# Optimization experiments

Hardware: AMD Instinct MI355X
Metric: run time of the kernel (lower is better)

The kernel has to match this reference:

```python
import jax, jax.numpy as jnp
import numpy as np

DIM = 768
HEADS = 12


def setup_inputs() -> dict:
    key = jax.random.key(0)
    ks = jax.random.split(key, 8)
    B, N, M, C, H = 8, 1024, 1024, DIM, HEADS
    x = jax.random.normal(ks[0], (B, N, C), dtype=jnp.float32)
    context = jax.random.normal(ks[1], (B, M, C), dtype=jnp.float32)
    s = 1.0 / np.sqrt(C)
    Wq = jax.random.normal(ks[2], (C, C), dtype=jnp.float32) * s
    Wkv = jax.random.normal(ks[3], (C, 2 * C), dtype=jnp.float32) * s
    # depthwise 3x3 conv over attention map: OIHW with I=1 (groups=H)
    conv_w = jax.random.normal(ks[4], (H, 1, 3, 3), dtype=jnp.float32) * (1.0 / 3.0)
    conv_b = jax.random.normal(ks[5], (H,), dtype=jnp.float32) * 0.02
    Wp = jax.random.normal(ks[6], (C, C), dtype=jnp.float32) * s
    bp = jax.random.normal(ks[7], (C,), dtype=jnp.float32) * 0.02
    return {"x": x, "context": context, "Wq": Wq, "Wkv": Wkv,
            "conv_w": conv_w, "conv_b": conv_b, "Wp": Wp, "bp": bp}


def reference(x, context, Wq, Wkv, conv_w, conv_b, Wp, bp):
    B, N, C = x.shape
    H = conv_w.shape[0]
    d = C // H
    scale = d ** (-0.5)
    # projections
    q = (x @ Wq).reshape(B, N, H, d).transpose(0, 2, 1, 3)          # [B,H,N,d]
    kv = (context @ Wkv).reshape(B, -1, 2, H, d)
    k = kv[:, :, 0].transpose(0, 2, 1, 3)                            # [B,H,M,d]
    v = kv[:, :, 1].transpose(0, 2, 1, 3)                            # [B,H,M,d]
    # attention scores + softmax over keys
    attn = jnp.einsum('bhnd,bhmd->bhnm', q, k) * scale               # [B,H,N,M]
    attn = jax.nn.softmax(attn, axis=-1)
    # depthwise 3x3 conv on the attention map (heads = channels)
    attn = jax.lax.conv_general_dilated(
        attn, conv_w, window_strides=(1, 1), padding='SAME',
        feature_group_count=H,
        dimension_numbers=('NCHW', 'OIHW', 'NCHW'))
    attn = attn + conv_b[None, :, None, None]
    # attend values, merge heads, output projection
    out = jnp.einsum('bhnm,bhmd->bhnd', attn, v)                     # [B,H,N,d]
    out = out.transpose(0, 2, 1, 3).reshape(B, N, C)
    return out @ Wp + bp
```

## Files before the change

### kernel.cpp

```cpp
#include <hip/hip_runtime.h>
#include <hip/hip_bf16.h>

typedef __hip_bfloat16 bf16;
typedef __hip_bfloat162 bf162;

#define B_ 8
#define N_ 1024
#define M_ 1024
#define C_ 768
#define H_ 12
#define D_ 64

typedef __attribute__((ext_vector_type(8))) short short8v;
typedef __attribute__((ext_vector_type(4))) float f32x4;

__device__ __forceinline__ float bf2f(bf16 v){ return __bfloat162float(v); }
__device__ __forceinline__ bf16 f2bf(float v){ return __float2bfloat16(v); }

__device__ __forceinline__ void gl_lds16(const bf16* g, bf16* l){
  __builtin_amdgcn_global_load_lds((const __attribute__((address_space(1))) unsigned*)g,
                                   (__attribute__((address_space(3))) unsigned*)l, 16, 0, 0);
}

__global__ __launch_bounds__(256)
void cvt_both(const float* __restrict__ x, const float* __restrict__ ctx,
              bf16* __restrict__ xb, bf16* __restrict__ ctxb){
  int i = blockIdx.x*256 + threadIdx.x;
  const float* src; bf16* dst; int j;
  if (i < 786432){ src = x;   dst = xb;   j = i; }
  else           { src = ctx; dst = ctxb; j = i - 786432; }
  const float4* ip = reinterpret_cast<const float4*>(src) + 2*(size_t)j;
  float4 a = ip[0], b = ip[1];
  union { uint4 u; bf16 h[8]; } pk;
  pk.h[0]=f2bf(a.x); pk.h[1]=f2bf(a.y); pk.h[2]=f2bf(a.z); pk.h[3]=f2bf(a.w);
  pk.h[4]=f2bf(b.x); pk.h[5]=f2bf(b.y); pk.h[6]=f2bf(b.z); pk.h[7]=f2bf(b.w);
  reinterpret_cast<uint4*>(dst)[j] = pk.u;
}

__global__ __launch_bounds__(256)
void transpose_all(const float* __restrict__ Wq, const float* __restrict__ Wkv,
                   const float* __restrict__ Wp,
                   bf16* __restrict__ Wqt, bf16* __restrict__ Wkvt, bf16* __restrict__ Wpt)
{
  __shared__ float tile[32][33];
  int bid = blockIdx.x;
  const float* W; bf16* Wt; int N, bx, by;
  if (bid < 576)       { W = Wq;  Wt = Wqt;  N = 768;  bx = bid % 24;  by = bid / 24; }
  else if (bid < 1728) { int r = bid - 576;  W = Wkv; Wt = Wkvt; N = 1536; bx = r % 48; by = r / 48; }
  else                 { int r = bid - 1728; W = Wp;  Wt = Wpt;  N = 768;  bx = r % 24; by = r / 24; }
  const int K = 768;
  const int n0 = bx*32, k0 = by*32;
  const int tx = threadIdx.x & 31, ty = threadIdx.x >> 5;
#pragma unroll
  for (int i=0;i<32;i+=8) tile[ty+i][tx] = W[(size_t)(k0+ty+i)*N + n0+tx];
  __syncthreads();
#pragma unroll
  for (int i=0;i<32;i+=8) Wt[(size_t)(n0+ty+i)*K + k0+tx] = f2bf(tile[tx][ty+i]);
}

__global__ __launch_bounds__(1024)
void yprep(bf16* __restrict__ Vt, bf16* __restrict__ Y0, bf16* __restrict__ Y1,
           float* __restrict__ SV, const float* __restrict__ conv_w)
{
  __shared__ bf16 sm[65536];
  const int t = threadIdx.x;
  const int bh = blockIdx.x;
  const int h = bh % H_;
  const size_t pbase = (size_t)bh * 65536;

  float w[9];
#pragma unroll
  for (int q=0;q<9;q++) w[q] = conv_w[h*9+q];

#pragma unroll
  for (int k=0;k<8;k++){
    int idx = k*8192 + t*8;
    *reinterpret_cast<uint4*>(&sm[idx]) = *reinterpret_cast<const uint4*>(Vt + pbase + idx);
  }
  __syncthreads();

  const int d = t >> 4;
  const int j = t & 15;
  const int xb = (d >> 1) & 3;
  float ssum = 0.f;
#pragma unroll
  for (int k=0;k<8;k++){
    const int moff = j*64 + k*8;
    const int base = d*1024 + moff;
    union { uint4 u; bf16 hh[8]; } mv;
    mv.u = *reinterpret_cast<const uint4*>(&sm[base]);
    float v[8];
#pragma unroll
    for (int e=0;e<8;e++) v[e] = bf2f(mv.hh[e]);
    float vl = (moff == 0)    ? 0.f : bf2f(sm[base-1]);
    float vr = (moff == 1016) ? 0.f : bf2f(sm[base+8]);

    union { uint4 u; bf16 hh[8]; } o0, o1, o2;
#pragma unroll
    for (int m=0;m<8;m++){
      float vm1 = (m==0) ? vl : v[m-1];
      float vp1 = (m==7) ? vr : v[m+1];
      o0.hh[m] = f2bf(w[0]*vp1 + w[1]*v[m] + w[2]*vm1);
      o1.hh[m] = f2bf(w[3]*vp1 + w[4]*v[m] + w[5]*vm1);
      o2.hh[m] = f2bf(w[6]*vp1 + w[7]*v[m] + w[8]*vm1);
      ssum += v[m];
    }
    const int blk = (moff >> 3) & 3;
    size_t go = pbase + ((size_t)(moff>>5)<<11) + d*32 + ((blk ^ xb)<<3);
    *reinterpret_cast<uint4*>(Y0 + go) = o0.u;
    *reinterpret_cast<uint4*>(Y1 + go) = o1.u;
    *reinterpret_cast<uint4*>(Vt + go) = o2.u;
  }

  ssum += __shfl_xor(ssum, 1);
  ssum += __shfl_xor(ssum, 2);
  ssum += __shfl_xor(ssum, 4);
  ssum += __shfl_xor(ssum, 8);
  if (j == 0) SV[bh*64 + d] = ssum;
}

__global__ __launch_bounds__(256)
void gemm_qkv(const bf16* __restrict__ A0, const bf16* __restrict__ A1,
              const bf16* __restrict__ Bt0, const bf16* __restrict__ Bt1,
              bf16* __restrict__ outQ, bf16* __restrict__ outK, bf16* __restrict__ outV)
{
  __shared__ bf16 As[128*32];
  __shared__ bf16 Bs[128*32];
  const int K = 768;

  const int nwg = 1152, cpx = nwg >> 3;
  int bid = blockIdx.x;
  bid = (bid & 7)*cpx + (bid >> 3);
  const int rowb = bid / 18, colb = bid - rowb*18;
  const int row0 = rowb*128;
  const bool isQ = (colb < 6);
  const int c0 = isQ ? colb*128 : (colb-6)*128;

  const int t = threadIdx.x;
  const int w = t>>6, l = t&63, lr = l&15, g = l>>4;
  const int wr = w>>1, wc = w&1;

  const bf16* Ap = (isQ ? A0 : A1) + (size_t)row0*K;
  const bf16* Bp = (isQ ? Bt0 : Bt1) + (size_t)c0*K;
  const int srow = t>>2;
  const int schunk = (t&3)*8;

  f32x4 acc[4][4];
#pragma unroll
  for (int mi=0;mi<4;mi++)
#pragma unroll
    for (int ni=0;ni<4;ni++) acc[mi][ni] = (f32x4){0.f,0.f,0.f,0.f};

  for (int k0 = 0; k0 < K; k0 += 32){
    gl_lds16(Ap + (size_t)srow*K      + k0 + schunk, As + t*8);
    gl_lds16(Ap + (size_t)(srow+64)*K + k0 + schunk, As + 2048 + t*8);
    gl_lds16(Bp + (size_t)srow*K      + k0 + schunk, Bs + t*8);
    gl_lds16(Bp + (size_t)(srow+64)*K + k0 + schunk, Bs + 2048 + t*8);
    __syncthreads();

    short8v a[4], b[4];
#pragma unroll
    for (int mi=0;mi<4;mi++)
      a[mi] = *reinterpret_cast<const short8v*>(&As[(wr*64+mi*16+lr)*32 + g*8]);
#pragma unroll
    for (int ni=0;ni<4;ni++)
      b[ni] = *reinterpret_cast<const short8v*>(&Bs[(wc*64+ni*16+lr)*32 + g*8]);
#pragma unroll
    for (int mi=0;mi<4;mi++)
#pragma unroll
      for (int ni=0;ni<4;ni++)
        acc[mi][ni] = __builtin_amdgcn_mfma_f32_16x16x32_bf16(a[mi], b[ni], acc[mi][ni], 0,0,0);
    __syncthreads();
  }

  if (isQ){
#pragma unroll
    for (int mi=0;mi<4;mi++)
#pragma unroll
      for (int ni=0;ni<4;ni++){
        int c = c0 + wc*64 + ni*16 + lr;
        int h = c >> 6, dd = c & 63;
#pragma unroll
        for (int q=0;q<4;q++){
          int grow = row0 + wr*64 + mi*16 + g*4 + q;
          int b = grow >> 10, n = grow & 1023;
          outQ[((((size_t)b*H_ + h)*N_ + n)<<6) + dd] = f2bf(acc[mi][ni][q] * 0.18033688f);
        }
      }
  } else {
#pragma unroll
    for (int mi=0;mi<4;mi++)
#pragma unroll
      for (int ni=0;ni<4;ni++){
        int c = c0 + wc*64 + ni*16 + lr;
        if (c < 768){
          int h = c >> 6, dd = c & 63;
#pragma unroll
          for (int q=0;q<4;q++){
            int grow = row0 + wr*64 + mi*16 + g*4 + q;
            int b = grow >> 10, m = grow & 1023;
            int eidx = ((m>>4)<<10) + ((dd>>3)<<7) + ((m&15)<<3) + (dd&7);
            outK[((size_t)b*H_ + h)*65536 + eidx] = f2bf(acc[mi][ni][q]);
          }
        } else {
          int cc = c - 768;
          int h = cc >> 6, dd = cc & 63;
          int grow = row0 + wr*64 + mi*16 + g*4;
          int b = grow >> 10, m = grow & 1023;
          union { ushort4 u; bf16 hh[4]; } pk;
#pragma unroll
          for (int q=0;q<4;q++) pk.hh[q] = f2bf(acc[mi][ni][q]);
          size_t off = (((size_t)b*H_ + h)*D_ + dd)*(size_t)M_ + m;
          *reinterpret_cast<ushort4*>(&outV[off]) = pk.u;
        }
      }
  }
}

__global__ __launch_bounds__(256)
void gemm_out(const bf16* __restrict__ A, const bf16* __restrict__ Bt,
              const float* __restrict__ bias, float* __restrict__ outf)
{
  __shared__ bf16 As[128*32];
  __shared__ bf16 Bs[128*32];
  const int K = 768;

  const int nwg = 384, cpx = nwg >> 3;
  int bid = blockIdx.x;
  bid = (bid & 7)*cpx + (bid >> 3);
  const int rowb = bid / 6, colb = bid - rowb*6;
  const int row0 = rowb*128, c0 = colb*128;

  const int t = threadIdx.x;
  const int w = t>>6, l = t&63, lr = l&15, g = l>>4;
  const int wr = w>>1, wc = w&1;

  const bf16* Ap = A + (size_t)row0*K;
  const bf16* Bp = Bt + (size_t)c0*K;
  const int srow = t>>2;
  const int schunk = (t&3)*8;

  f32x4 acc[4][4];
#pragma unroll
  for (int mi=0;mi<4;mi++)
#pragma unroll
    for (int ni=0;ni<4;ni++) acc[mi][ni] = (f32x4){0.f,0.f,0.f,0.f};

  for (int k0 = 0; k0 < K; k0 += 32){
    gl_lds16(Ap + (size_t)srow*K      + k0 + schunk, As + t*8);
    gl_lds16(Ap + (size_t)(srow+64)*K + k0 + schunk, As + 2048 + t*8);
    gl_lds16(Bp + (size_t)srow*K      + k0 + schunk, Bs + t*8);
    gl_lds16(Bp + (size_t)(srow+64)*K + k0 + schunk, Bs + 2048 + t*8);
    __syncthreads();

    short8v a[4], b[4];
#pragma unroll
    for (int mi=0;mi<4;mi++)
      a[mi] = *reinterpret_cast<const short8v*>(&As[(wr*64+mi*16+lr)*32 + g*8]);
#pragma unroll
    for (int ni=0;ni<4;ni++)
      b[ni] = *reinterpret_cast<const short8v*>(&Bs[(wc*64+ni*16+lr)*32 + g*8]);
#pragma unroll
    for (int mi=0;mi<4;mi++)
#pragma unroll
      for (int ni=0;ni<4;ni++)
        acc[mi][ni] = __builtin_amdgcn_mfma_f32_16x16x32_bf16(a[mi], b[ni], acc[mi][ni], 0,0,0);
    __syncthreads();
  }

  float bv[4];
#pragma unroll
  for (int ni=0;ni<4;ni++) bv[ni] = bias[c0 + wc*64 + ni*16 + lr];
#pragma unroll
  for (int mi=0;mi<4;mi++)
#pragma unroll
    for (int ni=0;ni<4;ni++){
      int c = c0 + wc*64 + ni*16 + lr;
#pragma unroll
      for (int q=0;q<4;q++){
        int grow = row0 + wr*64 + mi*16 + g*4 + q;
        outf[(size_t)grow*C_ + c] = acc[mi][ni][q] + bv[ni];
      }
    }
}

__global__ __launch_bounds__(512, 2)
void attn_coop(const bf16* __restrict__ Qb, const bf16* __restrict__ Kb,
               const bf16* __restrict__ Y0, const bf16* __restrict__ Y1,
               const bf16* __restrict__ Y2, const float* __restrict__ SV,
               const float* __restrict__ conv_b, bf16* __restrict__ midb,
               float* __restrict__ E0, float* __restrict__ E127,
               float* __restrict__ X0, float* __restrict__ X1)
{
  __shared__ bf16 sS[2][16384];
  __shared__ bf16 Psh[8192];
  float* linvs = reinterpret_cast<float*>(Psh);
  float* eU0   = linvs + 128;
  float* eU2   = eU0 + 256;
  bf16*  smOut = &sS[0][0];

  const int t = threadIdx.x, w = t>>6, l = t&63, lr = l&15, g = l>>4;
  const int qp = w & 3, dtp = w >> 2;
  int bid2 = (blockIdx.x & 7)*96 + (blockIdx.x >> 3);
  const int bh = bid2 >> 3, tile = bid2 & 7;
  const int b = bh / H_, h = bh - b*H_;
  const int n0 = tile*128;

  const bf16* Qp  = Qb + (size_t)bh*65536;
  const bf16* Kp  = Kb + (size_t)bh*65536;
  const bf16* Y0p = Y0 + (size_t)bh*65536;
  const bf16* Y1p = Y1 + (size_t)bh*65536;
  const bf16* Y2p = Y2 + (size_t)bh*65536;
  const float cbv = conv_b[h];

  const bf16* qpp = Qp + (size_t)(n0 + w*16 + lr)*D_ + g*8;
  short8v qf0 = *reinterpret_cast<const short8v*>(qpp);
  short8v qf1 = *reinterpret_cast<const short8v*>(qpp + 32);

  float lsum = 0.f;
  f32x4 U[2][3][2];
#pragma unroll
  for (int s2=0;s2<2;s2++)
#pragma unroll
    for (int y=0;y<3;y++)
#pragma unroll
      for (int dl=0;dl<2;dl++) U[s2][y][dl] = (f32x4){0.f,0.f,0.f,0.f};

  const int pkey = lr & 7;
  const int yswz = (lr >> 1) & 3;

  gl_lds16(Kp  + t*8, sS[0] + t*8);
  gl_lds16(Y0p + t*8, sS[0] + 4096  + t*8);
  gl_lds16(Y1p + t*8, sS[0] + 8192  + t*8);
  gl_lds16(Y2p + t*8, sS[0] + 12288 + t*8);

  for (int mc = 0; mc < 16; ++mc){
    const int cur = mc & 1;
    if (mc < 15){
      const size_t off = (size_t)(mc+1)*4096 + t*8;
      bf16* nb = sS[cur ^ 1];
      gl_lds16(Kp  + off, nb + t*8);
      gl_lds16(Y0p + off, nb + 4096  + t*8);
      gl_lds16(Y1p + off, nb + 8192  + t*8);
      gl_lds16(Y2p + off, nb + 12288 + t*8);
      asm volatile("s_waitcnt vmcnt(4)" ::: "memory");
    } else {
      asm volatile("s_waitcnt vmcnt(0)" ::: "memory");
    }
    __builtin_amdgcn_s_barrier();
    const bf16* sb = sS[cur];

    f32x4 s[4];
    __builtin_amdgcn_s_setprio(1);
#pragma unroll
    for (int st=0; st<4; ++st){
      const int ka = st*1024 + g*128 + lr*8;
      short8v k0 = *reinterpret_cast<const short8v*>(&sb[ka]);
      short8v k1 = *reinterpret_cast<const short8v*>(&sb[ka + 512]);
      f32x4 a = (f32x4){0.f,0.f,0.f,0.f};
      a = __builtin_amdgcn_mfma_f32_16x16x32_bf16(k0, qf0, a, 0,0,0);
      a = __builtin_amdgcn_mfma_f32_16x16x32_bf16(k1, qf1, a, 0,0,0);
      s[st] = a;
    }
    __builtin_amdgcn_s_setprio(0);

    float psum = 0.f;
#pragma unroll
    for (int st=0; st<4; ++st){
      union { ushort4 u; bf16 hh[4]; } pk;
#pragma unroll
      for (int q=0;q<4;q++){
        float p = exp2f(s[st][q]);
        psum += p;
        pk.hh[q] = f2bf(p);
      }
      const int gran = (st*2 + (g>>1)) ^ pkey;
      *reinterpret_cast<ushort4*>(&Psh[(w*16+lr)*64 + gran*8 + (g&1)*4]) = pk.u;
    }
    lsum += psum;
    __builtin_amdgcn_s_barrier();

    __builtin_amdgcn_s_setprio(1);
#pragma unroll
    for (int ks=0; ks<2; ++ks){
      const int agr = ((ks*4 + g) ^ pkey) << 3;
      short8v a0 = *reinterpret_cast<const short8v*>(&Psh[(qp*32      + lr)*64 + agr]);
      short8v a1 = *reinterpret_cast<const short8v*>(&Psh[(qp*32 + 16 + lr)*64 + agr]);
#pragma unroll
      for (int dl=0; dl<2; ++dl){
        const int dd = dtp*32 + dl*16 + lr;
        const int ya = ks*2048 + (dd<<5) + ((g ^ yswz)<<3);
        short8v b0 = *reinterpret_cast<const short8v*>(&sb[4096  + ya]);
        short8v b1 = *reinterpret_cast<const short8v*>(&sb[8192  + ya]);
        short8v b2 = *reinterpret_cast<const short8v*>(&sb[12288 + ya]);
        U[0][0][dl] = __builtin_amdgcn_mfma_f32_16x16x32_bf16(a0, b0, U[0][0][dl], 0,0,0);
        U[1][0][dl] = __builtin_amdgcn_mfma_f32_16x16x32_bf16(a1, b0, U[1][0][dl], 0,0,0);
        U[0][1][dl] = __builtin_amdgcn_mfma_f32_16x16x32_bf16(a0, b1, U[0][1][dl], 0,0,0);
        U[1][1][dl] = __builtin_amdgcn_mfma_f32_16x16x32_bf16(a1, b1, U[1][1][dl], 0,0,0);
        U[0][2][dl] = __builtin_amdgcn_mfma_f32_16x16x32_bf16(a0, b2, U[0][2][dl], 0,0,0);
        U[1][2][dl] = __builtin_amdgcn_mfma_f32_16x16x32_bf16(a1, b2, U[1][2][dl], 0,0,0);
      }
    }
    __builtin_amdgcn_s_setprio(0);
    __builtin_amdgcn_s_barrier();
  }

  lsum += __shfl_xor(lsum, 16);
  lsum += __shfl_xor(lsum, 32);
  if (g == 0) linvs[w*16 + lr] = 1.f / lsum;
  __syncthreads();

#pragma unroll
  for (int s2=0;s2<2;s2++){
    const f32x4 lv = *reinterpret_cast<const f32x4*>(&linvs[qp*32 + s2*16 + g*4]);
#pragma unroll
    for (int y=0;y<3;y++)
#pragma unroll
      for (int dl=0;dl<2;dl++)
#pragma unroll
        for (int q=0;q<4;q++) U[s2][y][dl][q] *= lv[q];
  }

  float sv[2];
#pragma unroll
  for (int dl=0;dl<2;dl++) sv[dl] = SV[bh*64 + dtp*32 + dl*16 + lr];

  if (g == 3){
#pragma unroll
    for (int dl=0;dl<2;dl++) eU0[qp*64 + dtp*32 + dl*16 + lr] = U[1][0][dl][3];
  }
  if (g == 0){
#pragma unroll
    for (int dl=0;dl<2;dl++) eU2[qp*64 + dtp*32 + dl*16 + lr] = U[0][2][dl][0];
  }
  __syncthreads();

#pragma unroll
  for (int dl=0; dl<2; ++dl){
    const int d = dtp*32 + dl*16 + lr;
    const float base = cbv*sv[dl];

    float d0s0 = __shfl(U[0][0][dl][3], (l - 16) & 63);
    float d0s1 = __shfl(U[1][0][dl][3], (l - 16) & 63);
    float u2w0 = __shfl(U[0][2][dl][0], (l + 16) & 63);
    float u2w1 = __shfl(U[1][2][dl][0], (l + 16) & 63);

    {
      float u0s = g ? d0s0 : (qp > 0 ? eU0[(qp-1)*64 + d] : 0.f);
      float u2s = (g < 3) ? u2w0 : u2w1;
      float o0 = u0s           + U[0][1][dl][0] + U[0][2][dl][1] + base;
      float o1 = U[0][0][dl][0] + U[0][1][dl][1] + U[0][2][dl][2] + base;
      float o2 = U[0][0][dl][1] + U[0][1][dl][2] + U[0][2][dl][3] + base;
      float o3 = U[0][0][dl][2] + U[0][1][dl][3] + u2s            + base;
      const int r0 = qp*32 + g*4;
      smOut[(r0+0)*64 + d] = f2bf(o0);
      smOut[(r0+1)*64 + d] = f2bf(o1);
      smOut[(r0+2)*64 + d] = f2bf(o2);
      smOut[(r0+3)*64 + d] = f2bf(o3);
    }
    {
      float u0s = g ? d0s1 : d0s0;
      float u2s = (g < 3) ? u2w1 : (qp < 3 ? eU2[(qp+1)*64 + d] : 0.f);
      float o0 = u0s           + U[1][1][dl][0] + U[1][2][dl][1] + base;
      float o1 = U[1][0][dl][0] + U[1][1][dl][1] + U[1][2][dl][2] + base;
      float o2 = U[1][0][dl][1] + U[1][1][dl][2] + U[1][2][dl][3] + base;
      float o3 = U[1][0][dl][2] + U[1][1][dl][3] + u2s            + base;
      const int r0 = qp*32 + 16 + g*4;
      smOut[(r0+0)*64 + d] = f2bf(o0);
      smOut[(r0+1)*64 + d] = f2bf(o1);
      smOut[(r0+2)*64 + d] = f2bf(o2);
      smOut[(r0+3)*64 + d] = f2bf(o3);
    }

    const int ei = (bh*8 + tile)*64 + d;
    if (qp == 0 && g == 0){
      E0[ei] = U[0][1][dl][0] + U[0][2][dl][1] + base;
      X1[ei] = U[0][2][dl][0];
    }
    if (qp == 3 && g == 3){
      E127[ei] = U[1][0][dl][2] + U[1][1][dl][3] + base;
      X0[ei]   = U[1][0][dl][3];
    }
  }
  __syncthreads();

  {
    const int row = t >> 2, seg = t & 3;
    const bf16* src = smOut + row*64 + seg*16;
    uint4 v0 = *reinterpret_cast<const uint4*>(src);
    uint4 v1 = *reinterpret_cast<const uint4*>(src + 8);
    bf16* dst = midb + ((size_t)b*N_ + n0 + row)*C_ + h*D_ + seg*16;
    *reinterpret_cast<uint4*>(dst)     = v0;
    *reinterpret_cast<uint4*>(dst + 8) = v1;
  }
}

__global__ __launch_bounds__(256)
void edge_patch(const float* __restrict__ E0, const float* __restrict__ E127,
                const float* __restrict__ X0, const float* __restrict__ X1,
                bf16* __restrict__ midb)
{
  int idx = blockIdx.x*256 + threadIdx.x;
  int d = idx & 63;
  int rs = (idx >> 6) & 1;
  int tile = (idx >> 7) & 7;
  int bh = idx >> 10;
  int b = bh / H_, h = bh - b*H_;
  int n0 = tile*128;
  float v; int n;
  if (rs == 0){
    v = E0[(bh*8+tile)*64 + d] + (tile > 0 ? X0[(bh*8+tile-1)*64 + d] : 0.f);
    n = n0;
  } else {
    v = E127[(bh*8+tile)*64 + d] + (tile < 7 ? X1[(bh*8+tile+1)*64 + d] : 0.f);
    n = n0 + 127;
  }
  midb[((size_t)b*N_ + n)*C_ + h*D_ + d] = f2bf(v);
}

extern "C" void kernel_launch(void* const* d_in, const int* in_sizes, int n_in,
                              void* d_out, int out_size, void* d_ws, size_t ws_size,
                              hipStream_t stream) {
  const float* x     = (const float*)d_in[0];
  const float* ctx   = (const float*)d_in[1];
  const float* Wq    = (const float*)d_in[2];
  const float* Wkv   = (const float*)d_in[3];
  const float* convw = (const float*)d_in[4];
  const float* convb = (const float*)d_in[5];
  const float* Wp    = (const float*)d_in[6];
  const float* bp    = (const float*)d_in[7];
  float* out = (float*)d_out;

  char* ws = (char*)d_ws;
  bf16* buf0 = (bf16*)(ws);
  bf16* Wqt  = (bf16*)(ws + 12582912);
  bf16* Wkvt = (bf16*)(ws + 13762560);
  bf16* Wpt  = (bf16*)(ws + 16121856);
  bf16* Qb   = (bf16*)(ws + 17301504);
  bf16* Kb   = (bf16*)(ws + 29884416);
  bf16* Vt   = (bf16*)(ws + 42467328);
  float* SVb = (float*)(ws + 55050240);
  float* E0  = (float*)(ws + 55074816);
  float* E127= (float*)(ws + 55271424);
  float* X0  = (float*)(ws + 55468032);
  float* X1  = (float*)(ws + 55664640);

  bf16* xb = (bf16*)d_out;
  bf16* Y0 = (bf16*)d_out;
  bf16* Y1 = (bf16*)((char*)d_out + 12582912);

  transpose_all<<<2304, 256, 0, stream>>>(Wq, Wkv, Wp, Wqt, Wkvt, Wpt);
  cvt_both<<<6144, 256, 0, stream>>>(x, ctx, xb, buf0);

  gemm_qkv<<<1152, 256, 0, stream>>>(xb, buf0, Wqt, Wkvt, Qb, Kb, Vt);

  yprep<<<96, 1024, 0, stream>>>(Vt, Y0, Y1, SVb, convw);

  attn_coop<<<768, 512, 0, stream>>>(Qb, Kb, Y0, Y1, Vt, SVb, convb, buf0,
                                     E0, E127, X0, X1);
  edge_patch<<<384, 256, 0, stream>>>(E0, E127, X0, X1, buf0);

  gemm_out<<<384, 256, 0, stream>>>(buf0, Wpt, bp, out);
}
```

Baseline: 177.8 us.

## Single-buffer attention LDS with staggered K/Y prefetch, merge prep kernels, pad yprep LDS

The attention kernel drops double buffering (64KB) for a single 48KB layout. The next K chunk is loaded after the score phase and the next Y chunks after the PV phase, so LDS per block shrinks and occupancy could rise, at the cost of less latency hiding and extra waits. The fp32-to-bf16 conversion and weight-transpose kernels are merged into one launch to save launch overhead. yprep pads its LDS rows to avoid bank conflicts, computes the V row sums in a separate pass, and writes output contiguously while reading the swizzled position from LDS.

```diff
diff --git a/kernel.cpp b/kernel.cpp
--- a/kernel.cpp
+++ b/kernel.cpp
@@ -10,6 +10,7 @@
 #define C_ 768
 #define H_ 12
 #define D_ 64
+#define YST 1032
 
 typedef __attribute__((ext_vector_type(8))) short short8v;
 typedef __attribute__((ext_vector_type(4))) float f32x4;
@@ -23,27 +24,28 @@
 }
 
 __global__ __launch_bounds__(256)
-void cvt_both(const float* __restrict__ x, const float* __restrict__ ctx,
-              bf16* __restrict__ xb, bf16* __restrict__ ctxb){
-  int i = blockIdx.x*256 + threadIdx.x;
-  const float* src; bf16* dst; int j;
-  if (i < 786432){ src = x;   dst = xb;   j = i; }
-  else           { src = ctx; dst = ctxb; j = i - 786432; }
-  const float4* ip = reinterpret_cast<const float4*>(src) + 2*(size_t)j;
-  float4 a = ip[0], b = ip[1];
-  union { uint4 u; bf16 h[8]; } pk;
-  pk.h[0]=f2bf(a.x); pk.h[1]=f2bf(a.y); pk.h[2]=f2bf(a.z); pk.h[3]=f2bf(a.w);
-  pk.h[4]=f2bf(b.x); pk.h[5]=f2bf(b.y); pk.h[6]=f2bf(b.z); pk.h[7]=f2bf(b.w);
-  reinterpret_cast<uint4*>(dst)[j] = pk.u;
-}
-
-__global__ __launch_bounds__(256)
-void transpose_all(const float* __restrict__ Wq, const float* __restrict__ Wkv,
-                   const float* __restrict__ Wp,
-                   bf16* __restrict__ Wqt, bf16* __restrict__ Wkvt, bf16* __restrict__ Wpt)
+void prep_all(const float* __restrict__ x, const float* __restrict__ ctx,
+              bf16* __restrict__ xb, bf16* __restrict__ ctxb,
+              const float* __restrict__ Wq, const float* __restrict__ Wkv,
+              const float* __restrict__ Wp,
+              bf16* __restrict__ Wqt, bf16* __restrict__ Wkvt, bf16* __restrict__ Wpt)
 {
   __shared__ float tile[32][33];
   int bid = blockIdx.x;
+  if (bid < 6144){
+    int i = bid*256 + threadIdx.x;
+    const float* src; bf16* dst; int j;
+    if (i < 786432){ src = x;   dst = xb;   j = i; }
+    else           { src = ctx; dst = ctxb; j = i - 786432; }
+    const float4* ip = reinterpret_cast<const float4*>(src) + 2*(size_t)j;
+    float4 a = ip[0], b = ip[1];
+    union { uint4 u; bf16 h[8]; } pk;
+    pk.h[0]=f2bf(a.x); pk.h[1]=f2bf(a.y); pk.h[2]=f2bf(a.z); pk.h[3]=f2bf(a.w);
+    pk.h[4]=f2bf(b.x); pk.h[5]=f2bf(b.y); pk.h[6]=f2bf(b.z); pk.h[7]=f2bf(b.w);
+    reinterpret_cast<uint4*>(dst)[j] = pk.u;
+    return;
+  }
+  bid -= 6144;
   const float* W; bf16* Wt; int N, bx, by;
   if (bid < 576)       { W = Wq;  Wt = Wqt;  N = 768;  bx = bid % 24;  by = bid / 24; }
   else if (bid < 1728) { int r = bid - 576;  W = Wkv; Wt = Wkvt; N = 1536; bx = r % 48; by = r / 48; }
@@ -62,7 +64,7 @@
 void yprep(bf16* __restrict__ Vt, bf16* __restrict__ Y0, bf16* __restrict__ Y1,
            float* __restrict__ SV, const float* __restrict__ conv_w)
 {
-  __shared__ bf16 sm[65536];
+  __shared__ bf16 sm[64*YST];
   const int t = threadIdx.x;
   const int bh = blockIdx.x;
   const int h = bh % H_;
@@ -75,25 +77,43 @@
 #pragma unroll
   for (int k=0;k<8;k++){
     int idx = k*8192 + t*8;
-    *reinterpret_cast<uint4*>(&sm[idx]) = *reinterpret_cast<const uint4*>(Vt + pbase + idx);
+    int d = idx >> 10, m = idx & 1023;
+    *reinterpret_cast<uint4*>(&sm[d*YST + m]) = *reinterpret_cast<const uint4*>(Vt + pbase + idx);
   }
   __syncthreads();
 
-  const int d = t >> 4;
-  const int j = t & 15;
-  const int xb = (d >> 1) & 3;
-  float ssum = 0.f;
+  {
+    const int d = t >> 4, j = t & 15;
+    float s = 0.f;
+#pragma unroll
+    for (int k=0;k<8;k++){
+      union { uint4 u; bf16 hh[8]; } mv;
+      mv.u = *reinterpret_cast<const uint4*>(&sm[d*YST + j*64 + k*8]);
+#pragma unroll
+      for (int e=0;e<8;e++) s += bf2f(mv.hh[e]);
+    }
+    s += __shfl_xor(s, 1); s += __shfl_xor(s, 2);
+    s += __shfl_xor(s, 4); s += __shfl_xor(s, 8);
+    if (j == 0) SV[bh*64 + d] = s;
+  }
+
+  const int d    = (t & 255) >> 2;
+  const int blkS = t & 3;
+  const int xb   = (d >> 1) & 3;
+  const int mbb  = t >> 8;
 #pragma unroll
   for (int k=0;k<8;k++){
-    const int moff = j*64 + k*8;
-    const int base = d*1024 + moff;
+    const int c  = k*1024 + t;
+    const int mb = k*4 + mbb;
+    const int m0 = mb*32 + ((blkS ^ xb) << 3);
+    const int base = d*YST + m0;
     union { uint4 u; bf16 hh[8]; } mv;
     mv.u = *reinterpret_cast<const uint4*>(&sm[base]);
     float v[8];
 #pragma unroll
     for (int e=0;e<8;e++) v[e] = bf2f(mv.hh[e]);
-    float vl = (moff == 0)    ? 0.f : bf2f(sm[base-1]);
-    float vr = (moff == 1016) ? 0.f : bf2f(sm[base+8]);
+    float vl = (m0 == 0)    ? 0.f : bf2f(sm[base-1]);
+    float vr = (m0 == 1016) ? 0.f : bf2f(sm[base+8]);
 
     union { uint4 u; bf16 hh[8]; } o0, o1, o2;
 #pragma unroll
@@ -103,20 +123,12 @@
       o0.hh[m] = f2bf(w[0]*vp1 + w[1]*v[m] + w[2]*vm1);
       o1.hh[m] = f2bf(w[3]*vp1 + w[4]*v[m] + w[5]*vm1);
       o2.hh[m] = f2bf(w[6]*vp1 + w[7]*v[m] + w[8]*vm1);
-      ssum += v[m];
-    }
-    const int blk = (moff >> 3) & 3;
-    size_t go = pbase + ((size_t)(moff>>5)<<11) + d*32 + ((blk ^ xb)<<3);
+    }
+    const size_t go = pbase + (size_t)c*8;
     *reinterpret_cast<uint4*>(Y0 + go) = o0.u;
     *reinterpret_cast<uint4*>(Y1 + go) = o1.u;
     *reinterpret_cast<uint4*>(Vt + go) = o2.u;
   }
-
-  ssum += __shfl_xor(ssum, 1);
-  ssum += __shfl_xor(ssum, 2);
-  ssum += __shfl_xor(ssum, 4);
-  ssum += __shfl_xor(ssum, 8);
-  if (j == 0) SV[bh*64 + d] = ssum;
 }
 
 __global__ __launch_bounds__(256)
@@ -292,12 +304,14 @@
                float* __restrict__ E0, float* __restrict__ E127,
                float* __restrict__ X0, float* __restrict__ X1)
 {
-  __shared__ bf16 sS[2][16384];
-  __shared__ bf16 Psh[8192];
-  float* linvs = reinterpret_cast<float*>(Psh);
+  __shared__ char smem[49152];
+  bf16* sK  = reinterpret_cast<bf16*>(smem);
+  bf16* sY  = reinterpret_cast<bf16*>(smem + 8192);
+  bf16* Psh = reinterpret_cast<bf16*>(smem + 32768);
+  bf16*  smOut = reinterpret_cast<bf16*>(smem);
+  float* linvs = reinterpret_cast<float*>(smem + 32768);
   float* eU0   = linvs + 128;
   float* eU2   = eU0 + 256;
-  bf16*  smOut = &sS[0][0];
 
   const int t = threadIdx.x, w = t>>6, l = t&63, lr = l&15, g = l>>4;
   const int qp = w & 3, dtp = w >> 2;
@@ -329,34 +343,21 @@
   const int pkey = lr & 7;
   const int yswz = (lr >> 1) & 3;
 
-  gl_lds16(Kp  + t*8, sS[0] + t*8);
-  gl_lds16(Y0p + t*8, sS[0] + 4096  + t*8);
-  gl_lds16(Y1p + t*8, sS[0] + 8192  + t*8);
-  gl_lds16(Y2p + t*8, sS[0] + 12288 + t*8);
+  gl_lds16(Kp  + t*8, sK + t*8);
+  gl_lds16(Y0p + t*8, sY + t*8);
+  gl_lds16(Y1p + t*8, sY + 4096 + t*8);
+  gl_lds16(Y2p + t*8, sY + 8192 + t*8);
+  asm volatile("s_waitcnt vmcnt(0)" ::: "memory");
+  __builtin_amdgcn_s_barrier();
 
   for (int mc = 0; mc < 16; ++mc){
-    const int cur = mc & 1;
-    if (mc < 15){
-      const size_t off = (size_t)(mc+1)*4096 + t*8;
-      bf16* nb = sS[cur ^ 1];
-      gl_lds16(Kp  + off, nb + t*8);
-      gl_lds16(Y0p + off, nb + 4096  + t*8);
-      gl_lds16(Y1p + off, nb + 8192  + t*8);
-      gl_lds16(Y2p + off, nb + 12288 + t*8);
-      asm volatile("s_waitcnt vmcnt(4)" ::: "memory");
-    } else {
-      asm volatile("s_waitcnt vmcnt(0)" ::: "memory");
-    }
-    __builtin_amdgcn_s_barrier();
-    const bf16* sb = sS[cur];
-
     f32x4 s[4];
     __builtin_amdgcn_s_setprio(1);
 #pragma unroll
     for (int st=0; st<4; ++st){
       const int ka = st*1024 + g*128 + lr*8;
-      short8v k0 = *reinterpret_cast<const short8v*>(&sb[ka]);
-      short8v k1 = *reinterpret_cast<const short8v*>(&sb[ka + 512]);
+      short8v k0 = *reinterpret_cast<const short8v*>(&sK[ka]);
+      short8v k1 = *reinterpret_cast<const short8v*>(&sK[ka + 512]);
       f32x4 a = (f32x4){0.f,0.f,0.f,0.f};
       a = __builtin_amdgcn_mfma_f32_16x16x32_bf16(k0, qf0, a, 0,0,0);
       a = __builtin_amdgcn_mfma_f32_16x16x32_bf16(k1, qf1, a, 0,0,0);
@@ -378,7 +379,11 @@
       *reinterpret_cast<ushort4*>(&Psh[(w*16+lr)*64 + gran*8 + (g&1)*4]) = pk.u;
     }
     lsum += psum;
+
+    asm volatile("s_waitcnt vmcnt(0) lgkmcnt(0)" ::: "memory");
     __builtin_amdgcn_s_barrier();
+
+    if (mc < 15) gl_lds16(Kp + (size_t)(mc+1)*4096 + t*8, sK + t*8);
 
     __builtin_amdgcn_s_setprio(1);
 #pragma unroll
@@ -390,9 +395,9 @@
       for (int dl=0; dl<2; ++dl){
         const int dd = dtp*32 + dl*16 + lr;
         const int ya = ks*2048 + (dd<<5) + ((g ^ yswz)<<3);
-        short8v b0 = *reinterpret_cast<const short8v*>(&sb[4096  + ya]);
-        short8v b1 = *reinterpret_cast<const short8v*>(&sb[8192  + ya]);
-        short8v b2 = *reinterpret_cast<const short8v*>(&sb[12288 + ya]);
+        short8v b0 = *reinterpret_cast<const short8v*>(&sY[ya]);
+        short8v b1 = *reinterpret_cast<const short8v*>(&sY[4096 + ya]);
+        short8v b2 = *reinterpret_cast<const short8v*>(&sY[8192 + ya]);
         U[0][0][dl] = __builtin_amdgcn_mfma_f32_16x16x32_bf16(a0, b0, U[0][0][dl], 0,0,0);
         U[1][0][dl] = __builtin_amdgcn_mfma_f32_16x16x32_bf16(a1, b0, U[1][0][dl], 0,0,0);
         U[0][1][dl] = __builtin_amdgcn_mfma_f32_16x16x32_bf16(a0, b1, U[0][1][dl], 0,0,0);
@@ -402,7 +407,16 @@
       }
     }
     __builtin_amdgcn_s_setprio(0);
+
+    asm volatile("s_waitcnt vmcnt(0)" ::: "memory");
     __builtin_amdgcn_s_barrier();
+
+    if (mc < 15){
+      const size_t off = (size_t)(mc+1)*4096 + t*8;
+      gl_lds16(Y0p + off, sY + t*8);
+      gl_lds16(Y1p + off, sY + 4096 + t*8);
+      gl_lds16(Y2p + off, sY + 8192 + t*8);
+    }
   }
 
   lsum += __shfl_xor(lsum, 16);
@@ -448,7 +462,7 @@
     {
       float u0s = g ? d0s0 : (qp > 0 ? eU0[(qp-1)*64 + d] : 0.f);
       float u2s = (g < 3) ? u2w0 : u2w1;
-      float o0 = u0s           + U[0][1][dl][0] + U[0][2][dl][1] + base;
+      float o0 = u0s            + U[0][1][dl][0] + U[0][2][dl][1] + base;
       float o1 = U[0][0][dl][0] + U[0][1][dl][1] + U[0][2][dl][2] + base;
       float o2 = U[0][0][dl][1] + U[0][1][dl][2] + U[0][2][dl][3] + base;
       float o3 = U[0][0][dl][2] + U[0][1][dl][3] + u2s            + base;
@@ -461,7 +475,7 @@
     {
       float u0s = g ? d0s1 : d0s0;
       float u2s = (g < 3) ? u2w1 : (qp < 3 ? eU2[(qp+1)*64 + d] : 0.f);
-      float o0 = u0s           + U[1][1][dl][0] + U[1][2][dl][1] + base;
+      float o0 = u0s            + U[1][1][dl][0] + U[1][2][dl][1] + base;
       float o1 = U[1][0][dl][0] + U[1][1][dl][1] + U[1][2][dl][2] + base;
       float o2 = U[1][0][dl][1] + U[1][1][dl][2] + U[1][2][dl][3] + base;
       float o3 = U[1][0][dl][2] + U[1][1][dl][3] + u2s            + base;
@@ -549,8 +563,7 @@
   bf16* Y0 = (bf16*)d_out;
   bf16* Y1 = (bf16*)((char*)d_out + 12582912);
 
-  transpose_all<<<2304, 256, 0, stream>>>(Wq, Wkv, Wp, Wqt, Wkvt, Wpt);
-  cvt_both<<<6144, 256, 0, stream>>>(x, ctx, xb, buf0);
+  prep_all<<<8448, 256, 0, stream>>>(x, ctx, xb, buf0, Wq, Wkv, Wp, Wqt, Wkvt, Wpt);
 
   gemm_qkv<<<1152, 256, 0, stream>>>(xb, buf0, Wqt, Wkvt, Qb, Kb, Vt);
 
```

Result: faster. 155.9 us, median of 3 (-12.4%).
